# Optimization experiments

Hardware: AMD Instinct MI355X
Metric: run time of the kernel (lower is better)

## Reference

```python
import jax, jax.numpy as jnp
import numpy as np

HEADS = 8
DIM_KEY = 256
NUM_KEYS = 256           # sqrt(num_experts)
PK_TOPK = 16             # product_key_topk (defaults to num_experts_per_head)
K_PER_HEAD = 16          # num_experts_per_head


def setup_inputs() -> dict:
    key = jax.random.key(0)
    k1, k2, k3, k4, k5 = jax.random.split(key, 5)
    b, n, d = 2, 1024, 512          # batch MUST be 2 (see module quirk)
    num_experts = NUM_KEYS * NUM_KEYS
    x = jax.random.normal(k1, (b, n, d), jnp.float32)
    Wq = jax.random.normal(k2, (2 * HEADS * DIM_KEY, d), jnp.float32) * 0.02
    keys = jax.random.normal(k3, (HEADS, NUM_KEYS, 2, DIM_KEY), jnp.float32)
    w_down = jax.random.normal(k4, (num_experts, d), jnp.float32) * 0.02
    w_up = jax.random.normal(k5, (num_experts, d), jnp.float32) * 0.02
    return {"x": x, "Wq": Wq, "keys": keys, "w_down": w_down, "w_up": w_up}


def reference(x, Wq, keys, w_down, w_up):
    b, n, d = x.shape  # b == 2 required by the original module's einsum/unpack
    # to_queries: Linear -> Unflatten(-1,(2,h,dk)) -> permute(0,2,1,3,4)
    q = (x @ Wq.T).reshape(b, n, 2, HEADS, DIM_KEY).transpose(0, 2, 1, 3, 4)  # (b,2,n,h,dk)
    kk = keys.transpose(2, 0, 1, 3)  # (2, h, num_keys, dk)
    # faithful to original: 'p' axis of queries is the BATCH axis (requires b==2)
    sim = jnp.einsum('pbnhd,phkd->pbnhk', q, kk)  # (2, 2, n, h, num_keys)
    sx, ix = jax.lax.top_k(sim[0], PK_TOPK)
    sy, iy = jax.lax.top_k(sim[1], PK_TOPK)
    # combine product keys: (2, n, h, T, T) -> (2, n, h, T*T)
    all_scores = (sx[..., :, None] + sy[..., None, :]).reshape(*sx.shape[:-1], PK_TOPK * PK_TOPK)
    all_indices = (ix[..., :, None] * NUM_KEYS + iy[..., None, :]).reshape(*ix.shape[:-1], PK_TOPK * PK_TOPK)
    scores, pk = jax.lax.top_k(all_scores, K_PER_HEAD)          # (2, n, h, K)
    indices = jnp.take_along_axis(all_indices, pk, axis=-1)     # (2, n, h, K)
    wd = w_down[indices]  # (2, n, h, K, d) huge gather
    wu = w_up[indices]    # (2, n, h, K, d)
    h = jnp.einsum('bnd,bnhkd->bnhk', x, wd)
    h = jax.nn.gelu(h, approximate=False)  # torch nn.GELU default = exact erf
    h = h * jax.nn.softmax(scores, axis=-1)
    return jnp.einsum('bnhk,bnhkd->bnd', h, wu)
```

## Files before the change

### kernel.cpp

```cpp
#include <hip/hip_runtime.h>
#include <hip/hip_bf16.h>
#include <math.h>

__device__ __forceinline__ unsigned f2u(float f) {
    unsigned b = __float_as_uint(f);
    return b ^ ((unsigned)((int)b >> 31) | 0x80000000u);
}
__device__ __forceinline__ float u2f(unsigned u) {
    unsigned b = (u & 0x80000000u) ? (u ^ 0x80000000u) : ~u;
    return __uint_as_float(b);
}
__device__ __forceinline__ unsigned short f2bf(float f) {
    unsigned b = __float_as_uint(f);
    return (unsigned short)((b + 0x7FFFu + ((b >> 16) & 1u)) >> 16);
}
__device__ __forceinline__ float bflo(unsigned u) { return __uint_as_float(u << 16); }
__device__ __forceinline__ float bfhi(unsigned u) { return __uint_as_float(u & 0xFFFF0000u); }

__device__ __forceinline__ void radix16(unsigned u0, unsigned u1, unsigned u2, unsigned u3,
                                        unsigned& T, int& kk) {
    unsigned prefix = 0; int k = 16;
    for (int b = 31; b >= 0; --b) {
        unsigned hi = (prefix >> b) | 1u;
        int cnt = __popcll(__ballot((u0 >> b) == hi))
                + __popcll(__ballot((u1 >> b) == hi))
                + __popcll(__ballot((u2 >> b) == hi))
                + __popcll(__ballot((u3 >> b) == hi));
        if (cnt >= k) prefix |= (1u << b); else k -= cnt;
    }
    T = prefix; kk = k;
}

__global__ __launch_bounds__(256) void k0_transpose(const float* __restrict__ keys,
                                                    float* __restrict__ KT) {
    int bid = blockIdx.x;
    int dt = bid & 3, ktile = (bid >> 2) & 3, p = (bid >> 4) & 1, h = bid >> 5;
    __shared__ float tile[64][65];
    int t = threadIdx.x;
    int row = t >> 2;
    int c4  = t & 3;
#pragma unroll
    for (int i = 0; i < 4; ++i) {
        int dloc = (c4 + 4 * i) * 4;
        float4 v = *(const float4*)&keys[(size_t)(((h * 256 + ktile * 64 + row) * 2 + p) * 256) + dt * 64 + dloc];
        tile[dloc + 0][row] = v.x;
        tile[dloc + 1][row] = v.y;
        tile[dloc + 2][row] = v.z;
        tile[dloc + 3][row] = v.w;
    }
    __syncthreads();
#pragma unroll
    for (int i = 0; i < 4; ++i) {
        int kloc = (c4 + 4 * i) * 4;
        float4 v;
        v.x = tile[row][kloc]; v.y = tile[row][kloc + 1];
        v.z = tile[row][kloc + 2]; v.w = tile[row][kloc + 3];
        *(float4*)&KT[(size_t)((h * 2 + p) * 256 + dt * 64 + row) * 256 + ktile * 64 + kloc] = v;
    }
}

__global__ __launch_bounds__(256) void k_conv(const float* __restrict__ src,
                                              unsigned short* __restrict__ dst, int n8) {
    int tid = blockIdx.x * 256 + threadIdx.x;
    int stride = gridDim.x * 256;
    for (int i = tid; i < n8; i += stride) {
        float4 a = *(const float4*)&src[(size_t)i * 8];
        float4 b = *(const float4*)&src[(size_t)i * 8 + 4];
        uint4 o;
        o.x = (unsigned)f2bf(a.x) | ((unsigned)f2bf(a.y) << 16);
        o.y = (unsigned)f2bf(a.z) | ((unsigned)f2bf(a.w) << 16);
        o.z = (unsigned)f2bf(b.x) | ((unsigned)f2bf(b.y) << 16);
        o.w = (unsigned)f2bf(b.z) | ((unsigned)f2bf(b.w) << 16);
        *(uint4*)&dst[(size_t)i * 8] = o;
    }
}

__global__ __launch_bounds__(256) void k1_gemm(const float* __restrict__ A,
                                               const float* __restrict__ B,
                                               float* __restrict__ C) {
    __shared__ float As[16][128];
    __shared__ float Bs[16][128];
    int t  = threadIdx.x;
    int tx = t & 15, ty = t >> 4;
    int m0 = blockIdx.y * 128, n0 = blockIdx.x * 128;
    float acc[8][8] = {};
    for (int k0 = 0; k0 < 512; k0 += 16) {
#pragma unroll
        for (int i = 0; i < 2; ++i) {
            int u   = t * 2 + i;
            int row = u >> 2;
            int kc  = (u & 3) << 2;
            float4 av = *(const float4*)&A[(m0 + row) * 512 + k0 + kc];
            float4 bv = *(const float4*)&B[(n0 + row) * 512 + k0 + kc];
            As[kc + 0][row] = av.x; As[kc + 1][row] = av.y; As[kc + 2][row] = av.z; As[kc + 3][row] = av.w;
            Bs[kc + 0][row] = bv.x; Bs[kc + 1][row] = bv.y; Bs[kc + 2][row] = bv.z; Bs[kc + 3][row] = bv.w;
        }
        __syncthreads();
#pragma unroll
        for (int kk = 0; kk < 16; ++kk) {
            float4 a0 = *(const float4*)&As[kk][ty * 8];
            float4 a1 = *(const float4*)&As[kk][ty * 8 + 4];
            float4 b0 = *(const float4*)&Bs[kk][tx * 8];
            float4 b1 = *(const float4*)&Bs[kk][tx * 8 + 4];
            float a[8] = {a0.x, a0.y, a0.z, a0.w, a1.x, a1.y, a1.z, a1.w};
            float b[8] = {b0.x, b0.y, b0.z, b0.w, b1.x, b1.y, b1.z, b1.w};
#pragma unroll
            for (int i = 0; i < 8; ++i)
#pragma unroll
                for (int j = 0; j < 8; ++j) acc[i][j] += a[i] * b[j];
        }
        __syncthreads();
    }
#pragma unroll
    for (int i = 0; i < 8; ++i) {
        int m = m0 + ty * 8 + i;
        float4 o0; o0.x = acc[i][0]; o0.y = acc[i][1]; o0.z = acc[i][2]; o0.w = acc[i][3];
        float4 o1; o1.x = acc[i][4]; o1.y = acc[i][5]; o1.z = acc[i][6]; o1.w = acc[i][7];
        *(float4*)&C[m * 4096 + n0 + tx * 8]     = o0;
        *(float4*)&C[m * 4096 + n0 + tx * 8 + 4] = o1;
    }
}

__global__ __launch_bounds__(512) void k2_scores(const float* __restrict__ q,
                                                 const float* __restrict__ KT,
                                                 int* __restrict__ widx,
                                                 float* __restrict__ wcoef) {
    int bid = blockIdx.x;
    int cc = bid & 1;
    int h  = (bid >> 1) & 7;
    int n0 = (bid >> 4) * 16;

    __shared__ float sx_s[2][16][16];
    __shared__ int   ix_s[2][16][16];

    int t = threadIdx.x;
    int wv = t >> 6, ln = t & 63;
    int wvu = __builtin_amdgcn_readfirstlane(wv);
    int pu  = wvu >> 2;
    int nq  = wvu & 3;
    unsigned long long lt = (1ull << ln) - 1ull;

    const float* qw = q + ((size_t)(pu * 1024 + n0 + nq * 4) * 4096 + cc * 2048 + h * 256);
    const float* kp = KT + (size_t)((h * 2 + pu) * 256) * 256 + 4 * ln;

    float acc[4][4];
#pragma unroll
    for (int n = 0; n < 4; ++n)
#pragma unroll
        for (int j = 0; j < 4; ++j) acc[n][j] = 0.f;

    for (int d0 = 0; d0 < 256; d0 += 8) {
        float4 kt[8];
#pragma unroll
        for (int dd = 0; dd < 8; ++dd)
            kt[dd] = *(const float4*)&kp[(size_t)(d0 + dd) * 256];
#pragma unroll
        for (int n = 0; n < 4; ++n) {
            float4 qa = *(const float4*)&qw[(size_t)n * 4096 + d0];
            float4 qb = *(const float4*)&qw[(size_t)n * 4096 + d0 + 4];
            acc[n][0] += qa.x * kt[0].x + qa.y * kt[1].x + qa.z * kt[2].x + qa.w * kt[3].x
                       + qb.x * kt[4].x + qb.y * kt[5].x + qb.z * kt[6].x + qb.w * kt[7].x;
            acc[n][1] += qa.x * kt[0].y + qa.y * kt[1].y + qa.z * kt[2].y + qa.w * kt[3].y
                       + qb.x * kt[4].y + qb.y * kt[5].y + qb.z * kt[6].y + qb.w * kt[7].y;
            acc[n][2] += qa.x * kt[0].z + qa.y * kt[1].z + qa.z * kt[2].z + qa.w * kt[3].z
                       + qb.x * kt[4].z + qb.y * kt[5].z + qb.z * kt[6].z + qb.w * kt[7].z;
            acc[n][3] += qa.x * kt[0].w + qa.y * kt[1].w + qa.z * kt[2].w + qa.w * kt[3].w
                       + qb.x * kt[4].w + qb.y * kt[5].w + qb.z * kt[6].w + qb.w * kt[7].w;
        }
    }

#pragma unroll
    for (int n = 0; n < 4; ++n) {
        int nn = nq * 4 + n;
        unsigned u0 = f2u(acc[n][0]), u1 = f2u(acc[n][1]);
        unsigned u2 = f2u(acc[n][2]), u3 = f2u(acc[n][3]);
        unsigned T; int kk;
        radix16(u0, u1, u2, u3, T, kk);
        int base = 0;
#define TK1_GT(J, UJ, VJ) { unsigned long long m = __ballot(UJ > T);            \
        if (UJ > T) { int pos = base + __popcll(m & lt);                        \
            sx_s[pu][nn][pos] = VJ; ix_s[pu][nn][pos] = ln * 4 + J; }           \
        base += __popcll(m); }
        TK1_GT(0, u0, acc[n][0]); TK1_GT(1, u1, acc[n][1]);
        TK1_GT(2, u2, acc[n][2]); TK1_GT(3, u3, acc[n][3]);
#undef TK1_GT
#define TK1_EQ(J, UJ, VJ) { unsigned long long m = __ballot(UJ == T);           \
        int r = __popcll(m & lt);                                               \
        if ((UJ == T) && r < kk) { sx_s[pu][nn][base + r] = VJ;                 \
            ix_s[pu][nn][base + r] = ln * 4 + J; }                              \
        int cn = __popcll(m); int tk = cn < kk ? cn : kk;                       \
        base += tk; kk -= tk; }
        TK1_EQ(0, u0, acc[n][0]); TK1_EQ(1, u1, acc[n][1]);
        TK1_EQ(2, u2, acc[n][2]); TK1_EQ(3, u3, acc[n][3]);
#undef TK1_EQ
    }
    __syncthreads();

    for (int task = wv * 2; task < wv * 2 + 2; ++task) {
        int n = task;
        int t0 = ln, t1 = ln + 64, t2 = ln + 128, t3 = ln + 192;
        float vc0 = sx_s[0][n][t0 >> 4] + sx_s[1][n][t0 & 15];
        float vc1 = sx_s[0][n][t1 >> 4] + sx_s[1][n][t1 & 15];
        float vc2 = sx_s[0][n][t2 >> 4] + sx_s[1][n][t2 & 15];
        float vc3 = sx_s[0][n][t3 >> 4] + sx_s[1][n][t3 & 15];
        unsigned u0 = f2u(vc0), u1 = f2u(vc1), u2 = f2u(vc2), u3 = f2u(vc3);
        unsigned T; int kk;
        radix16(u0, u1, u2, u3, T, kk);
        float Tf = u2f(T);

        bool w0 = u0 > T, w1 = u1 > T, w2 = u2 > T, w3 = u3 > T;
        int q0 = 0, q1 = 0, q2 = 0, q3 = 0;
        int base = 0;
        { unsigned long long m = __ballot(w0); q0 = base + __popcll(m & lt); base += __popcll(m); }
        { unsigned long long m = __ballot(w1); q1 = base + __popcll(m & lt); base += __popcll(m); }
        { unsigned long long m = __ballot(w2); q2 = base + __popcll(m & lt); base += __popcll(m); }
        { unsigned long long m = __ballot(w3); q3 = base + __popcll(m & lt); base += __popcll(m); }
#define CMB_EQ(UJ, WJ, QJ) { unsigned long long m = __ballot(UJ == T);          \
        int r = __popcll(m & lt);                                               \
        if ((UJ == T) && r < kk) { WJ = true; QJ = base + r; }                  \
        int cn = __popcll(m); int tk = cn < kk ? cn : kk;                       \
        base += tk; kk -= tk; }
        CMB_EQ(u0, w0, q0); CMB_EQ(u1, w1, q1); CMB_EQ(u2, w2, q2); CMB_EQ(u3, w3, q3);
#undef CMB_EQ

        float e0 = 0.f, e1 = 0.f, e2 = 0.f, e3 = 0.f;
        int id0 = 0, id1 = 0, id2 = 0, id3 = 0;
        float es = 0.f;
        if (w0) { e0 = __expf(vc0 - Tf); es += e0; id0 = ix_s[0][n][t0 >> 4] * 256 + ix_s[1][n][t0 & 15]; }
        if (w1) { e1 = __expf(vc1 - Tf); es += e1; id1 = ix_s[0][n][t1 >> 4] * 256 + ix_s[1][n][t1 & 15]; }
        if (w2) { e2 = __expf(vc2 - Tf); es += e2; id2 = ix_s[0][n][t2 >> 4] * 256 + ix_s[1][n][t2 & 15]; }
        if (w3) { e3 = __expf(vc3 - Tf); es += e3; id3 = ix_s[0][n][t3 >> 4] * 256 + ix_s[1][n][t3 & 15]; }
        for (int s = 1; s < 64; s <<= 1) es += __shfl_xor(es, s);
        float inv = 1.f / es;

        int off = ((cc * 1024 + n0 + n) * 8 + h) * 16;
        if (w0) { wcoef[off + q0] = e0 * inv; widx[off + q0] = id0; }
        if (w1) { wcoef[off + q1] = e1 * inv; widx[off + q1] = id1; }
        if (w2) { wcoef[off + q2] = e2 * inv; widx[off + q2] = id2; }
        if (w3) { wcoef[off + q3] = e3 * inv; widx[off + q3] = id3; }
    }
}

__global__ __launch_bounds__(256) void k3_experts_bf16(const float* __restrict__ x,
                                                       const unsigned short* __restrict__ wd,
                                                       const unsigned short* __restrict__ wu,
                                                       const int* __restrict__ widx,
                                                       const float* __restrict__ wcoef,
                                                       float* __restrict__ out) {
    int bid = blockIdx.x;
    int c = bid >> 10, n = bid & 1023;
    int t = threadIdx.x, wv = t >> 6, ln = t & 63;
    __shared__ float wacc[4][512];

    const float* xrow = &x[(c * 1024 + n) * 512];
    float xr[8], oacc[8];
    {
        float4 xa = *(const float4*)&xrow[ln * 8];
        float4 xb = *(const float4*)&xrow[ln * 8 + 4];
        xr[0] = xa.x; xr[1] = xa.y; xr[2] = xa.z; xr[3] = xa.w;
        xr[4] = xb.x; xr[5] = xb.y; xr[6] = xb.z; xr[7] = xb.w;
    }
#pragma unroll
    for (int j = 0; j < 8; ++j) oacc[j] = 0.f;

    const int base = (c * 1024 + n) * 128;
    for (int e = wv * 32; e < wv * 32 + 32; ++e) {
        int   idx = widx[base + e];
        float wgt = wcoef[base + e];
        uint4 dv = *(const uint4*)&wd[(size_t)idx * 512 + ln * 8];
        float part = bflo(dv.x) * xr[0] + bfhi(dv.x) * xr[1]
                   + bflo(dv.y) * xr[2] + bfhi(dv.y) * xr[3]
                   + bflo(dv.z) * xr[4] + bfhi(dv.z) * xr[5]
                   + bflo(dv.w) * xr[6] + bfhi(dv.w) * xr[7];
        for (int s = 1; s < 64; s <<= 1) part += __shfl_xor(part, s);
        float hv = part;
        float coef = 0.5f * hv * (1.f + erff(hv * 0.70710678118654752f)) * wgt;
        uint4 uv = *(const uint4*)&wu[(size_t)idx * 512 + ln * 8];
        oacc[0] += coef * bflo(uv.x); oacc[1] += coef * bfhi(uv.x);
        oacc[2] += coef * bflo(uv.y); oacc[3] += coef * bfhi(uv.y);
        oacc[4] += coef * bflo(uv.z); oacc[5] += coef * bfhi(uv.z);
        oacc[6] += coef * bflo(uv.w); oacc[7] += coef * bfhi(uv.w);
    }

#pragma unroll
    for (int j = 0; j < 8; ++j) wacc[wv][ln * 8 + j] = oacc[j];
    __syncthreads();

    float* orow = &out[(c * 1024 + n) * 512];
    for (int d = t; d < 512; d += 256)
        orow[d] = wacc[0][d] + wacc[1][d] + wacc[2][d] + wacc[3][d];
}

__global__ __launch_bounds__(256) void k3_experts_f32(const float* __restrict__ x,
                                                      const float* __restrict__ w_down,
                                                      const float* __restrict__ w_up,
                                                      const int* __restrict__ widx,
                                                      const float* __restrict__ wcoef,
                                                      float* __restrict__ out) {
    int bid = blockIdx.x;
    int c = bid >> 10, n = bid & 1023;
    int t = threadIdx.x, wv = t >> 6, ln = t & 63;
    __shared__ float wacc[4][512];

    const float* xrow = &x[(c * 1024 + n) * 512];
    float xr[8], oacc[8];
    {
        float4 xa = *(const float4*)&xrow[ln * 8];
        float4 xb = *(const float4*)&xrow[ln * 8 + 4];
        xr[0] = xa.x; xr[1] = xa.y; xr[2] = xa.z; xr[3] = xa.w;
        xr[4] = xb.x; xr[5] = xb.y; xr[6] = xb.z; xr[7] = xb.w;
    }
#pragma unroll
    for (int j = 0; j < 8; ++j) oacc[j] = 0.f;

    const int base = (c * 1024 + n) * 128;
    for (int e = wv * 32; e < wv * 32 + 32; ++e) {
        int   idx = widx[base + e];
        float wgt = wcoef[base + e];
        const float* dr = &w_down[(long)idx * 512 + ln * 8];
        float4 da = *(const float4*)&dr[0];
        float4 db = *(const float4*)&dr[4];
        float part = da.x * xr[0] + da.y * xr[1] + da.z * xr[2] + da.w * xr[3]
                   + db.x * xr[4] + db.y * xr[5] + db.z * xr[6] + db.w * xr[7];
        for (int s = 1; s < 64; s <<= 1) part += __shfl_xor(part, s);
        float hv = part;
        float coef = 0.5f * hv * (1.f + erff(hv * 0.70710678118654752f)) * wgt;
        const float* ur = &w_up[(long)idx * 512 + ln * 8];
        float4 ua = *(const float4*)&ur[0];
        float4 ub = *(const float4*)&ur[4];
        oacc[0] += coef * ua.x; oacc[1] += coef * ua.y; oacc[2] += coef * ua.z; oacc[3] += coef * ua.w;
        oacc[4] += coef * ub.x; oacc[5] += coef * ub.y; oacc[6] += coef * ub.z; oacc[7] += coef * ub.w;
    }
#pragma unroll
    for (int j = 0; j < 8; ++j) wacc[wv][ln * 8 + j] = oacc[j];
    __syncthreads();

    float* orow = &out[(c * 1024 + n) * 512];
    for (int d = t; d < 512; d += 256)
        orow[d] = wacc[0][d] + wacc[1][d] + wacc[2][d] + wacc[3][d];
}

extern "C" void kernel_launch(void* const* d_in, const int* in_sizes, int n_in,
                              void* d_out, int out_size, void* d_ws, size_t ws_size,
                              hipStream_t stream) {
    const float* x      = (const float*)d_in[0];
    const float* Wq     = (const float*)d_in[1];
    const float* keys   = (const float*)d_in[2];
    const float* w_down = (const float*)d_in[3];
    const float* w_up   = (const float*)d_in[4];
    float* out = (float*)d_out;

    char* ws = (char*)d_ws;
    size_t off = 0;
    float* q     = (float*)(ws + off); off += 2048UL * 4096 * 4;
    int*   widx  = (int*)(ws + off);   off += 262144UL * 4;
    float* wcoef = (float*)(ws + off); off += 262144UL * 4;
    float* KT    = (float*)(ws + off); off += 8UL * 2 * 256 * 256 * 4;
    unsigned short* wd16 = (unsigned short*)(ws + off); off += 65536UL * 512 * 2;
    unsigned short* wu16 = (unsigned short*)(ws + off); off += 65536UL * 512 * 2;
    bool use_bf16 = (ws_size >= off);

    k0_transpose<<<256, 256, 0, stream>>>(keys, KT);
    k1_gemm<<<dim3(32, 16), 256, 0, stream>>>(x, Wq, q);
    k2_scores<<<1024, 512, 0, stream>>>(q, KT, widx, wcoef);
    if (use_bf16) {
        k_conv<<<2048, 256, 0, stream>>>(w_down, wd16, 65536 * 512 / 8);
        k_conv<<<2048, 256, 0, stream>>>(w_up,   wu16, 65536 * 512 / 8);
        k3_experts_bf16<<<2048, 256, 0, stream>>>(x, wd16, wu16, widx, wcoef, out);
    } else {
        k3_experts_f32<<<2048, 256, 0, stream>>>(x, w_down, w_up, widx, wcoef, out);
    }
}
```

Before: 362.0 us.

## Fold product keys into Wq so scores come from one GEMM against x

Reassociates the query projection and key similarity. A first GEMM multiplies keys by Wq per head, half and p to form K2 (4096x512 per p), then x is multiplied by K2 to produce the scores directly. The old q projection followed by a separate per-head score kernel goes away, and top-k becomes a standalone one-wave-per-(c,n,h) kernel reading the precomputed scores. The FLOP count of the score path roughly halves, at the cost of a 2x larger effective GEMM and slightly different fp32 rounding order.

```diff
diff --git a/kernel.cpp b/kernel.cpp
--- a/kernel.cpp
+++ b/kernel.cpp
@@ -29,34 +29,6 @@
         if (cnt >= k) prefix |= (1u << b); else k -= cnt;
     }
     T = prefix; kk = k;
-}
-
-__global__ __launch_bounds__(256) void k0_transpose(const float* __restrict__ keys,
-                                                    float* __restrict__ KT) {
-    int bid = blockIdx.x;
-    int dt = bid & 3, ktile = (bid >> 2) & 3, p = (bid >> 4) & 1, h = bid >> 5;
-    __shared__ float tile[64][65];
-    int t = threadIdx.x;
-    int row = t >> 2;
-    int c4  = t & 3;
-#pragma unroll
-    for (int i = 0; i < 4; ++i) {
-        int dloc = (c4 + 4 * i) * 4;
-        float4 v = *(const float4*)&keys[(size_t)(((h * 256 + ktile * 64 + row) * 2 + p) * 256) + dt * 64 + dloc];
-        tile[dloc + 0][row] = v.x;
-        tile[dloc + 1][row] = v.y;
-        tile[dloc + 2][row] = v.z;
-        tile[dloc + 3][row] = v.w;
-    }
-    __syncthreads();
-#pragma unroll
-    for (int i = 0; i < 4; ++i) {
-        int kloc = (c4 + 4 * i) * 4;
-        float4 v;
-        v.x = tile[row][kloc]; v.y = tile[row][kloc + 1];
-        v.z = tile[row][kloc + 2]; v.w = tile[row][kloc + 3];
-        *(float4*)&KT[(size_t)((h * 2 + p) * 256 + dt * 64 + row) * 256 + ktile * 64 + kloc] = v;
-    }
 }
 
 __global__ __launch_bounds__(256) void k_conv(const float* __restrict__ src,
@@ -75,25 +47,34 @@
     }
 }
 
-__global__ __launch_bounds__(256) void k1_gemm(const float* __restrict__ A,
-                                               const float* __restrict__ B,
-                                               float* __restrict__ C) {
+__global__ __launch_bounds__(256) void kK2(const float* __restrict__ keys,
+                                           const float* __restrict__ Wq,
+                                           float* __restrict__ K2) {
     __shared__ float As[16][128];
     __shared__ float Bs[16][128];
     int t  = threadIdx.x;
     int tx = t & 15, ty = t >> 4;
-    int m0 = blockIdx.y * 128, n0 = blockIdx.x * 128;
+    int p = blockIdx.z;
+    int ktile = blockIdx.y & 1, ch = blockIdx.y >> 1;
+    int h = ch & 7, c = ch >> 3;
+    int m0 = ktile * 128;
+    int n0 = blockIdx.x * 128;
+    const float* kb = keys + ((size_t)(h * 256 + m0) * 2 + p) * 256;
+    const float* wb = Wq + (size_t)(c * 2048 + h * 256) * 512;
     float acc[8][8] = {};
-    for (int k0 = 0; k0 < 512; k0 += 16) {
+    for (int k0 = 0; k0 < 256; k0 += 16) {
 #pragma unroll
         for (int i = 0; i < 2; ++i) {
             int u   = t * 2 + i;
             int row = u >> 2;
             int kc  = (u & 3) << 2;
-            float4 av = *(const float4*)&A[(m0 + row) * 512 + k0 + kc];
-            float4 bv = *(const float4*)&B[(n0 + row) * 512 + k0 + kc];
+            float4 av = *(const float4*)&kb[(size_t)row * 512 + k0 + kc];
             As[kc + 0][row] = av.x; As[kc + 1][row] = av.y; As[kc + 2][row] = av.z; As[kc + 3][row] = av.w;
-            Bs[kc + 0][row] = bv.x; Bs[kc + 1][row] = bv.y; Bs[kc + 2][row] = bv.z; Bs[kc + 3][row] = bv.w;
+            int v = u;
+            int dkrow = v >> 5;
+            int dcol  = (v & 31) << 2;
+            float4 bv = *(const float4*)&wb[(size_t)(k0 + dkrow) * 512 + n0 + dcol];
+            *(float4*)&Bs[dkrow][dcol] = bv;
         }
         __syncthreads();
 #pragma unroll
@@ -111,134 +92,169 @@
         }
         __syncthreads();
     }
+    float* Cp = K2 + (size_t)p * 4096 * 512;
+#pragma unroll
+    for (int i = 0; i < 8; ++i) {
+        int r = c * 2048 + h * 256 + m0 + ty * 8 + i;
+        float4 o0; o0.x = acc[i][0]; o0.y = acc[i][1]; o0.z = acc[i][2]; o0.w = acc[i][3];
+        float4 o1; o1.x = acc[i][4]; o1.y = acc[i][5]; o1.z = acc[i][6]; o1.w = acc[i][7];
+        *(float4*)&Cp[(size_t)r * 512 + n0 + tx * 8]     = o0;
+        *(float4*)&Cp[(size_t)r * 512 + n0 + tx * 8 + 4] = o1;
+    }
+}
+
+__global__ __launch_bounds__(256) void kS_gemm(const float* __restrict__ x,
+                                               const float* __restrict__ K2,
+                                               float* __restrict__ S) {
+    __shared__ float As[16][128];
+    __shared__ float Bs[16][128];
+    int t  = threadIdx.x;
+    int tx = t & 15, ty = t >> 4;
+    int p  = blockIdx.z;
+    int m0 = blockIdx.y * 128, n0 = blockIdx.x * 128;
+    const float* A = x  + (size_t)p * 1024 * 512;
+    const float* B = K2 + (size_t)p * 4096 * 512;
+    float* C = S + (size_t)p * 1024 * 4096;
+    float acc[8][8] = {};
+    for (int k0 = 0; k0 < 512; k0 += 16) {
+#pragma unroll
+        for (int i = 0; i < 2; ++i) {
+            int u   = t * 2 + i;
+            int row = u >> 2;
+            int kc  = (u & 3) << 2;
+            float4 av = *(const float4*)&A[(size_t)(m0 + row) * 512 + k0 + kc];
+            float4 bv = *(const float4*)&B[(size_t)(n0 + row) * 512 + k0 + kc];
+            As[kc + 0][row] = av.x; As[kc + 1][row] = av.y; As[kc + 2][row] = av.z; As[kc + 3][row] = av.w;
+            Bs[kc + 0][row] = bv.x; Bs[kc + 1][row] = bv.y; Bs[kc + 2][row] = bv.z; Bs[kc + 3][row] = bv.w;
+        }
+        __syncthreads();
+#pragma unroll
+        for (int kk = 0; kk < 16; ++kk) {
+            float4 a0 = *(const float4*)&As[kk][ty * 8];
+            float4 a1 = *(const float4*)&As[kk][ty * 8 + 4];
+            float4 b0 = *(const float4*)&Bs[kk][tx * 8];
+            float4 b1 = *(const float4*)&Bs[kk][tx * 8 + 4];
+            float a[8] = {a0.x, a0.y, a0.z, a0.w, a1.x, a1.y, a1.z, a1.w};
+            float b[8] = {b0.x, b0.y, b0.z, b0.w, b1.x, b1.y, b1.z, b1.w};
+#pragma unroll
+            for (int i = 0; i < 8; ++i)
+#pragma unroll
+                for (int j = 0; j < 8; ++j) acc[i][j] += a[i] * b[j];
+        }
+        __syncthreads();
+    }
 #pragma unroll
     for (int i = 0; i < 8; ++i) {
         int m = m0 + ty * 8 + i;
         float4 o0; o0.x = acc[i][0]; o0.y = acc[i][1]; o0.z = acc[i][2]; o0.w = acc[i][3];
         float4 o1; o1.x = acc[i][4]; o1.y = acc[i][5]; o1.z = acc[i][6]; o1.w = acc[i][7];
-        *(float4*)&C[m * 4096 + n0 + tx * 8]     = o0;
-        *(float4*)&C[m * 4096 + n0 + tx * 8 + 4] = o1;
-    }
-}
-
-__global__ __launch_bounds__(512) void k2_scores(const float* __restrict__ q,
-                                                 const float* __restrict__ KT,
-                                                 int* __restrict__ widx,
-                                                 float* __restrict__ wcoef) {
-    int bid = blockIdx.x;
-    int cc = bid & 1;
-    int h  = (bid >> 1) & 7;
-    int n0 = (bid >> 4) * 16;
-
-    __shared__ float sx_s[2][16][16];
-    __shared__ int   ix_s[2][16][16];
+        *(float4*)&C[(size_t)m * 4096 + n0 + tx * 8]     = o0;
+        *(float4*)&C[(size_t)m * 4096 + n0 + tx * 8 + 4] = o1;
+    }
+}
+
+__global__ __launch_bounds__(256) void k2_topk(const float* __restrict__ S,
+                                               int* __restrict__ widx,
+                                               float* __restrict__ wcoef) {
+    __shared__ float sx_s[4][2][16];
+    __shared__ int   ix_s[4][2][16];
 
     int t = threadIdx.x;
     int wv = t >> 6, ln = t & 63;
-    int wvu = __builtin_amdgcn_readfirstlane(wv);
-    int pu  = wvu >> 2;
-    int nq  = wvu & 3;
+    int task = blockIdx.x * 4 + wv;
+    int c = task >> 13;
+    int n = (task >> 3) & 1023;
+    int h = task & 7;
     unsigned long long lt = (1ull << ln) - 1ull;
 
-    const float* qw = q + ((size_t)(pu * 1024 + n0 + nq * 4) * 4096 + cc * 2048 + h * 256);
-    const float* kp = KT + (size_t)((h * 2 + pu) * 256) * 256 + 4 * ln;
-
-    float acc[4][4];
-#pragma unroll
-    for (int n = 0; n < 4; ++n)
-#pragma unroll
-        for (int j = 0; j < 4; ++j) acc[n][j] = 0.f;
-
-    for (int d0 = 0; d0 < 256; d0 += 8) {
-        float4 kt[8];
-#pragma unroll
-        for (int dd = 0; dd < 8; ++dd)
-            kt[dd] = *(const float4*)&kp[(size_t)(d0 + dd) * 256];
-#pragma unroll
-        for (int n = 0; n < 4; ++n) {
-            float4 qa = *(const float4*)&qw[(size_t)n * 4096 + d0];
-            float4 qb = *(const float4*)&qw[(size_t)n * 4096 + d0 + 4];
-            acc[n][0] += qa.x * kt[0].x + qa.y * kt[1].x + qa.z * kt[2].x + qa.w * kt[3].x
-                       + qb.x * kt[4].x + qb.y * kt[5].x + qb.z * kt[6].x + qb.w * kt[7].x;
-            acc[n][1] += qa.x * kt[0].y + qa.y * kt[1].y + qa.z * kt[2].y + qa.w * kt[3].y
-                       + qb.x * kt[4].y + qb.y * kt[5].y + qb.z * kt[6].y + qb.w * kt[7].y;
-            acc[n][2] += qa.x * kt[0].z + qa.y * kt[1].z + qa.z * kt[2].z + qa.w * kt[3].z
-                       + qb.x * kt[4].z + qb.y * kt[5].z + qb.z * kt[6].z + qb.w * kt[7].z;
-            acc[n][3] += qa.x * kt[0].w + qa.y * kt[1].w + qa.z * kt[2].w + qa.w * kt[3].w
-                       + qb.x * kt[4].w + qb.y * kt[5].w + qb.z * kt[6].w + qb.w * kt[7].w;
-        }
-    }
-
-#pragma unroll
-    for (int n = 0; n < 4; ++n) {
-        int nn = nq * 4 + n;
-        unsigned u0 = f2u(acc[n][0]), u1 = f2u(acc[n][1]);
-        unsigned u2 = f2u(acc[n][2]), u3 = f2u(acc[n][3]);
-        unsigned T; int kk;
-        radix16(u0, u1, u2, u3, T, kk);
-        int base = 0;
-#define TK1_GT(J, UJ, VJ) { unsigned long long m = __ballot(UJ > T);            \
-        if (UJ > T) { int pos = base + __popcll(m & lt);                        \
-            sx_s[pu][nn][pos] = VJ; ix_s[pu][nn][pos] = ln * 4 + J; }           \
-        base += __popcll(m); }
-        TK1_GT(0, u0, acc[n][0]); TK1_GT(1, u1, acc[n][1]);
-        TK1_GT(2, u2, acc[n][2]); TK1_GT(3, u3, acc[n][3]);
-#undef TK1_GT
-#define TK1_EQ(J, UJ, VJ) { unsigned long long m = __ballot(UJ == T);           \
-        int r = __popcll(m & lt);                                               \
-        if ((UJ == T) && r < kk) { sx_s[pu][nn][base + r] = VJ;                 \
-            ix_s[pu][nn][base + r] = ln * 4 + J; }                              \
-        int cn = __popcll(m); int tk = cn < kk ? cn : kk;                       \
-        base += tk; kk -= tk; }
-        TK1_EQ(0, u0, acc[n][0]); TK1_EQ(1, u1, acc[n][1]);
-        TK1_EQ(2, u2, acc[n][2]); TK1_EQ(3, u3, acc[n][3]);
-#undef TK1_EQ
-    }
+    const float* s0p = S + (size_t)n * 4096 + c * 2048 + h * 256 + ln * 4;
+    float4 s0 = *(const float4*)&s0p[0];
+    float4 s1 = *(const float4*)&s0p[1024UL * 4096];
+
+#define TK_HALF(PIDX, V)                                                          \
+    {                                                                             \
+        unsigned u0 = f2u(V.x), u1 = f2u(V.y), u2 = f2u(V.z), u3 = f2u(V.w);      \
+        unsigned T; int kk;                                                       \
+        radix16(u0, u1, u2, u3, T, kk);                                           \
+        int base = 0;                                                             \
+        { unsigned long long m = __ballot(u0 > T);                                \
+          if (u0 > T) { int pos = base + __popcll(m & lt);                        \
+              sx_s[wv][PIDX][pos] = V.x; ix_s[wv][PIDX][pos] = ln * 4 + 0; }      \
+          base += __popcll(m); }                                                  \
+        { unsigned long long m = __ballot(u1 > T);                                \
+          if (u1 > T) { int pos = base + __popcll(m & lt);                        \
+              sx_s[wv][PIDX][pos] = V.y; ix_s[wv][PIDX][pos] = ln * 4 + 1; }      \
+          base += __popcll(m); }                                                  \
+        { unsigned long long m = __ballot(u2 > T);                                \
+          if (u2 > T) { int pos = base + __popcll(m & lt);                        \
+              sx_s[wv][PIDX][pos] = V.z; ix_s[wv][PIDX][pos] = ln * 4 + 2; }      \
+          base += __popcll(m); }                                                  \
+        { unsigned long long m = __ballot(u3 > T);                                \
+          if (u3 > T) { int pos = base + __popcll(m & lt);                        \
+              sx_s[wv][PIDX][pos] = V.w; ix_s[wv][PIDX][pos] = ln * 4 + 3; }      \
+          base += __popcll(m); }                                                  \
+        { unsigned long long m = __ballot(u0 == T); int r = __popcll(m & lt);     \
+          if ((u0 == T) && r < kk) { sx_s[wv][PIDX][base + r] = V.x;              \
+              ix_s[wv][PIDX][base + r] = ln * 4 + 0; }                            \
+          int cn2 = __popcll(m); int tk = cn2 < kk ? cn2 : kk; base += tk; kk -= tk; } \
+        { unsigned long long m = __ballot(u1 == T); int r = __popcll(m & lt);     \
+          if ((u1 == T) && r < kk) { sx_s[wv][PIDX][base + r] = V.y;              \
+              ix_s[wv][PIDX][base + r] = ln * 4 + 1; }                            \
+          int cn2 = __popcll(m); int tk = cn2 < kk ? cn2 : kk; base += tk; kk -= tk; } \
+        { unsigned long long m = __ballot(u2 == T); int r = __popcll(m & lt);     \
+          if ((u2 == T) && r < kk) { sx_s[wv][PIDX][base + r] = V.z;              \
+              ix_s[wv][PIDX][base + r] = ln * 4 + 2; }                            \
+          int cn2 = __popcll(m); int tk = cn2 < kk ? cn2 : kk; base += tk; kk -= tk; } \
+        { unsigned long long m = __ballot(u3 == T); int r = __popcll(m & lt);     \
+          if ((u3 == T) && r < kk) { sx_s[wv][PIDX][base + r] = V.w;              \
+              ix_s[wv][PIDX][base + r] = ln * 4 + 3; }                            \
+          int cn2 = __popcll(m); int tk = cn2 < kk ? cn2 : kk; base += tk; kk -= tk; } \
+    }
+    TK_HALF(0, s0);
+    TK_HALF(1, s1);
+#undef TK_HALF
     __syncthreads();
 
-    for (int task = wv * 2; task < wv * 2 + 2; ++task) {
-        int n = task;
-        int t0 = ln, t1 = ln + 64, t2 = ln + 128, t3 = ln + 192;
-        float vc0 = sx_s[0][n][t0 >> 4] + sx_s[1][n][t0 & 15];
-        float vc1 = sx_s[0][n][t1 >> 4] + sx_s[1][n][t1 & 15];
-        float vc2 = sx_s[0][n][t2 >> 4] + sx_s[1][n][t2 & 15];
-        float vc3 = sx_s[0][n][t3 >> 4] + sx_s[1][n][t3 & 15];
-        unsigned u0 = f2u(vc0), u1 = f2u(vc1), u2 = f2u(vc2), u3 = f2u(vc3);
-        unsigned T; int kk;
-        radix16(u0, u1, u2, u3, T, kk);
-        float Tf = u2f(T);
-
-        bool w0 = u0 > T, w1 = u1 > T, w2 = u2 > T, w3 = u3 > T;
-        int q0 = 0, q1 = 0, q2 = 0, q3 = 0;
-        int base = 0;
-        { unsigned long long m = __ballot(w0); q0 = base + __popcll(m & lt); base += __popcll(m); }
-        { unsigned long long m = __ballot(w1); q1 = base + __popcll(m & lt); base += __popcll(m); }
-        { unsigned long long m = __ballot(w2); q2 = base + __popcll(m & lt); base += __popcll(m); }
-        { unsigned long long m = __ballot(w3); q3 = base + __popcll(m & lt); base += __popcll(m); }
+    int t0 = ln, t1 = ln + 64, t2 = ln + 128, t3 = ln + 192;
+    float vc0 = sx_s[wv][0][t0 >> 4] + sx_s[wv][1][t0 & 15];
+    float vc1 = sx_s[wv][0][t1 >> 4] + sx_s[wv][1][t1 & 15];
+    float vc2 = sx_s[wv][0][t2 >> 4] + sx_s[wv][1][t2 & 15];
+    float vc3 = sx_s[wv][0][t3 >> 4] + sx_s[wv][1][t3 & 15];
+    unsigned u0 = f2u(vc0), u1 = f2u(vc1), u2 = f2u(vc2), u3 = f2u(vc3);
+    unsigned T; int kk;
+    radix16(u0, u1, u2, u3, T, kk);
+    float Tf = u2f(T);
+
+    bool w0 = u0 > T, w1 = u1 > T, w2 = u2 > T, w3 = u3 > T;
+    int q0 = 0, q1 = 0, q2 = 0, q3 = 0;
+    int base = 0;
+    { unsigned long long m = __ballot(w0); q0 = base + __popcll(m & lt); base += __popcll(m); }
+    { unsigned long long m = __ballot(w1); q1 = base + __popcll(m & lt); base += __popcll(m); }
+    { unsigned long long m = __ballot(w2); q2 = base + __popcll(m & lt); base += __popcll(m); }
+    { unsigned long long m = __ballot(w3); q3 = base + __popcll(m & lt); base += __popcll(m); }
 #define CMB_EQ(UJ, WJ, QJ) { unsigned long long m = __ballot(UJ == T);          \
-        int r = __popcll(m & lt);                                               \
-        if ((UJ == T) && r < kk) { WJ = true; QJ = base + r; }                  \
-        int cn = __popcll(m); int tk = cn < kk ? cn : kk;                       \
-        base += tk; kk -= tk; }
-        CMB_EQ(u0, w0, q0); CMB_EQ(u1, w1, q1); CMB_EQ(u2, w2, q2); CMB_EQ(u3, w3, q3);
+    int r = __popcll(m & lt);                                                   \
+    if ((UJ == T) && r < kk) { WJ = true; QJ = base + r; }                      \
+    int cn2 = __popcll(m); int tk = cn2 < kk ? cn2 : kk;                        \
+    base += tk; kk -= tk; }
+    CMB_EQ(u0, w0, q0); CMB_EQ(u1, w1, q1); CMB_EQ(u2, w2, q2); CMB_EQ(u3, w3, q3);
 #undef CMB_EQ
 
-        float e0 = 0.f, e1 = 0.f, e2 = 0.f, e3 = 0.f;
-        int id0 = 0, id1 = 0, id2 = 0, id3 = 0;
-        float es = 0.f;
-        if (w0) { e0 = __expf(vc0 - Tf); es += e0; id0 = ix_s[0][n][t0 >> 4] * 256 + ix_s[1][n][t0 & 15]; }
-        if (w1) { e1 = __expf(vc1 - Tf); es += e1; id1 = ix_s[0][n][t1 >> 4] * 256 + ix_s[1][n][t1 & 15]; }
-        if (w2) { e2 = __expf(vc2 - Tf); es += e2; id2 = ix_s[0][n][t2 >> 4] * 256 + ix_s[1][n][t2 & 15]; }
-        if (w3) { e3 = __expf(vc3 - Tf); es += e3; id3 = ix_s[0][n][t3 >> 4] * 256 + ix_s[1][n][t3 & 15]; }
-        for (int s = 1; s < 64; s <<= 1) es += __shfl_xor(es, s);
-        float inv = 1.f / es;
-
-        int off = ((cc * 1024 + n0 + n) * 8 + h) * 16;
-        if (w0) { wcoef[off + q0] = e0 * inv; widx[off + q0] = id0; }
-        if (w1) { wcoef[off + q1] = e1 * inv; widx[off + q1] = id1; }
-        if (w2) { wcoef[off + q2] = e2 * inv; widx[off + q2] = id2; }
-        if (w3) { wcoef[off + q3] = e3 * inv; widx[off + q3] = id3; }
-    }
+    float e0 = 0.f, e1 = 0.f, e2 = 0.f, e3 = 0.f;
+    int id0 = 0, id1 = 0, id2 = 0, id3 = 0;
+    float es = 0.f;
+    if (w0) { e0 = __expf(vc0 - Tf); es += e0; id0 = ix_s[wv][0][t0 >> 4] * 256 + ix_s[wv][1][t0 & 15]; }
+    if (w1) { e1 = __expf(vc1 - Tf); es += e1; id1 = ix_s[wv][0][t1 >> 4] * 256 + ix_s[wv][1][t1 & 15]; }
+    if (w2) { e2 = __expf(vc2 - Tf); es += e2; id2 = ix_s[wv][0][t2 >> 4] * 256 + ix_s[wv][1][t2 & 15]; }
+    if (w3) { e3 = __expf(vc3 - Tf); es += e3; id3 = ix_s[wv][0][t3 >> 4] * 256 + ix_s[wv][1][t3 & 15]; }
+    for (int s = 1; s < 64; s <<= 1) es += __shfl_xor(es, s);
+    float inv = 1.f / es;
+
+    int off = ((c * 1024 + n) * 8 + h) * 16;
+    if (w0) { wcoef[off + q0] = e0 * inv; widx[off + q0] = id0; }
+    if (w1) { wcoef[off + q1] = e1 * inv; widx[off + q1] = id1; }
+    if (w2) { wcoef[off + q2] = e2 * inv; widx[off + q2] = id2; }
+    if (w3) { wcoef[off + q3] = e3 * inv; widx[off + q3] = id3; }
 }
 
 __global__ __launch_bounds__(256) void k3_experts_bf16(const float* __restrict__ x,
@@ -352,17 +368,17 @@
 
     char* ws = (char*)d_ws;
     size_t off = 0;
-    float* q     = (float*)(ws + off); off += 2048UL * 4096 * 4;
+    float* S     = (float*)(ws + off); off += 2048UL * 4096 * 4;
     int*   widx  = (int*)(ws + off);   off += 262144UL * 4;
     float* wcoef = (float*)(ws + off); off += 262144UL * 4;
-    float* KT    = (float*)(ws + off); off += 8UL * 2 * 256 * 256 * 4;
+    float* K2    = (float*)(ws + off); off += 2UL * 4096 * 512 * 4;
     unsigned short* wd16 = (unsigned short*)(ws + off); off += 65536UL * 512 * 2;
     unsigned short* wu16 = (unsigned short*)(ws + off); off += 65536UL * 512 * 2;
     bool use_bf16 = (ws_size >= off);
 
-    k0_transpose<<<256, 256, 0, stream>>>(keys, KT);
-    k1_gemm<<<dim3(32, 16), 256, 0, stream>>>(x, Wq, q);
-    k2_scores<<<1024, 512, 0, stream>>>(q, KT, widx, wcoef);
+    kK2<<<dim3(4, 32, 2), 256, 0, stream>>>(keys, Wq, K2);
+    kS_gemm<<<dim3(32, 8, 2), 256, 0, stream>>>(x, K2, S);
+    k2_topk<<<4096, 256, 0, stream>>>(S, widx, wcoef);
     if (use_bf16) {
         k_conv<<<2048, 256, 0, stream>>>(w_down, wd16, 65536 * 512 / 8);
         k_conv<<<2048, 256, 0, stream>>>(w_up,   wu16, 65536 * 512 / 8);
```

Result: faster. 347.3 us (-4.0%).
